# Optimization experiments

Hardware: AMD Instinct MI355X
Metric: run time of the kernel (lower is better)

Reference implementation:

```python
import jax, jax.numpy as jnp
import numpy as np

N = 100000        # nodes
E = 1600000       # edges
F_IN = 128        # input features
H = 64            # hidden
B = 256           # graphs in batch
MIN_SCORE = 1e-3  # SAGPooling min_score
TOL = 1e-7        # PyG topk tolerance
NEG = jnp.float32(-1e30)


def setup_inputs() -> dict:
    key = jax.random.key(0)
    ks = jax.random.split(key, 24)
    x = jax.random.normal(ks[0], (N, F_IN), jnp.float32)
    src = jax.random.randint(ks[1], (E,), 0, N, dtype=jnp.int32)
    dst = jax.random.randint(ks[2], (E,), 0, N, dtype=jnp.int32)
    batch = jnp.sort(jax.random.randint(ks[3], (N,), 0, B, dtype=jnp.int32))
    node_attention = jax.random.uniform(ks[4], (N,), jnp.float32)

    def lin(k, i, o):
        return jax.random.normal(k, (i, o), jnp.float32) / np.float32(np.sqrt(i))

    p = {
        'W11': lin(ks[5], F_IN, H), 'b11': jnp.zeros((H,), jnp.float32),
        'W12': lin(ks[6], H, H),    'b12': jnp.zeros((H,), jnp.float32),
        'gW1': lin(ks[7], H, 1),    'gb1': jnp.zeros((1,), jnp.float32),
        'W21': lin(ks[8], H, H),    'b21': jnp.zeros((H,), jnp.float32),
        'W22': lin(ks[9], H, H),    'b22': jnp.zeros((H,), jnp.float32),
        'gW2': lin(ks[10], H, 1),   'gb2': jnp.zeros((1,), jnp.float32),
        'W31': lin(ks[11], H, H),   'b31': jnp.zeros((H,), jnp.float32),
        'W32': lin(ks[12], H, H),   'b32': jnp.zeros((H,), jnp.float32),
        'Wl':  lin(ks[13], H, 1),   'bl': jnp.zeros((1,), jnp.float32),
    }
    return dict(x=x, src=src, dst=dst, batch=batch, node_attention=node_attention, **p)


def gin_conv(x, src, dst, emask, W1, b1, W2, b2):
    # GINConv, eps=0: mlp(x + sum_{j in N(i)} x_j), edges masked by emask
    agg = jax.ops.segment_sum(x[src] * emask[:, None], dst, num_segments=N)
    h = x + agg
    return jax.nn.relu(h @ W1 + b1) @ W2 + b2


def gcn_attn(x, src, dst, emask, nmask, W, b):
    # GCNConv(H,1) with self-loops + symmetric normalization on the masked graph
    h = x @ W  # [N,1]
    deg = jax.ops.segment_sum(emask, dst, num_segments=N) + nmask
    dinv = jnp.where(deg > 0, jax.lax.rsqrt(jnp.maximum(deg, 1e-12)), 0.0)
    coef = dinv[src] * dinv[dst] * emask
    out = jax.ops.segment_sum(h[src] * coef[:, None], dst, num_segments=N)
    out = out + h * (dinv * dinv * nmask)[:, None] + b
    return out[:, 0]


def seg_softmax(a, batch, nmask):
    am = jnp.where(nmask > 0, a, NEG)
    m = jax.ops.segment_max(am, batch, num_segments=B)
    e = jnp.where(nmask > 0, jnp.exp(a - m[batch]), 0.0)
    s = jax.ops.segment_sum(e, batch, num_segments=B)
    return e / jnp.maximum(s[batch], 1e-30)


def sag_pool(x, src, dst, emask, nmask, batch, W, b):
    attn = gcn_attn(x, src, dst, emask, nmask, W, b)
    score = seg_softmax(attn, batch, nmask)
    smax = jax.ops.segment_max(jnp.where(nmask > 0, score, NEG), batch, num_segments=B)
    thr = jnp.minimum(MIN_SCORE, smax[batch] - TOL)
    keep = ((nmask > 0) & (score > thr)).astype(x.dtype)
    x2 = x * (score * keep)[:, None]          # x[perm] * score[perm], masked form
    emask2 = emask * keep[src] * keep[dst]    # filter_adj
    return x2, emask2, keep, score


def reference(x, src, dst, batch, node_attention,
              W11, b11, W12, b12, gW1, gb1,
              W21, b21, W22, b22, gW2, gb2,
              W31, b31, W32, b32, Wl, bl):
    emask = jnp.ones((E,), x.dtype)
    nmask0 = jnp.ones((N,), x.dtype)

    h = jax.nn.relu(gin_conv(x, src, dst, emask, W11, b11, W12, b12))
    h, emask, keep1, _ = sag_pool(h, src, dst, emask, nmask0, batch, gW1, gb1)

    h = jax.nn.relu(gin_conv(h, src, dst, emask, W21, b21, W22, b22))
    h, emask, keep2, score2 = sag_pool(h, src, dst, emask, keep1, batch, gW2, gb2)

    ratio = jnp.sum(keep2) / jnp.float32(N)

    h = jax.nn.relu(gin_conv(h, src, dst, emask, W31, b31, W32, b32))

    # global max pool over surviving nodes
    hm = jnp.where(keep2[:, None] > 0, h, NEG)
    g = jax.ops.segment_max(hm, batch, num_segments=B)
    out = g @ Wl + bl  # [B,1]

    # attention KL loss; perm2 indexes the pool1-compacted array (as in the source)
    r1 = jnp.clip(jnp.cumsum(keep1).astype(jnp.int32) - 1, 0, N - 1)
    t = node_attention[r1]
    logp = jnp.log(score2 + 1e-14)
    kl = jnp.where(t > 0, t * jnp.log(jnp.maximum(t, 1e-38)), 0.0) - t * logp
    kl = kl * keep2
    s = jax.ops.segment_sum(kl, batch, num_segments=B)
    c = jax.ops.segment_sum(keep2, batch, num_segments=B)
    attn_loss = s / jnp.maximum(c, 1.0)  # scatter_mean

    return out, attn_loss, ratio
```

## Files before the change

kernel.cpp:

```cpp
#include <hip/hip_runtime.h>
#include <hip/hip_fp16.h>
#include <math.h>

#define NN 100000
#define NE 1600000
#define NB 256
#define NEGF (-1e30f)
#define NSCAN_BLK ((NN + 1023) / 1024)
#define GVB 1024
#define P_SORT 256
#define NBKT 391
#define HLEN (NBKT * P_SORT)
#define HSCAN_BLK ((HLEN + 1023) / 1024)
#define BKT_CAP 6144

__global__ void k_offs_bs(const int* __restrict__ batch, int* __restrict__ offs) {
    int g = blockIdx.x * 256 + threadIdx.x;
    if (g > NB) return;
    int lo = 0, hi = NN;
    while (lo < hi) { int mid = (lo + hi) >> 1; if (batch[mid] < g) lo = mid + 1; else hi = mid; }
    offs[g] = lo;
}

__global__ void k_hist_coarse(const int* __restrict__ dst, int* __restrict__ H) {
    __shared__ int lh[NBKT];
    int p = blockIdx.x, tid = threadIdx.x;
    for (int i = tid; i < NBKT; i += 256) lh[i] = 0;
    __syncthreads();
    int c0 = p * (NE / P_SORT), c1 = c0 + NE / P_SORT;
    for (int i = c0 + tid; i < c1; i += 256) atomicAdd(&lh[dst[i] >> 8], 1);
    __syncthreads();
    for (int i = tid; i < NBKT; i += 256) H[i * P_SORT + p] = lh[i];
}
__global__ void k_iscan_blk(const int* __restrict__ in, int* __restrict__ pref,
                            int* __restrict__ bsums, int len) {
    int blk = blockIdx.x, tid = threadIdx.x;
    int base = blk * 1024;
    int vals[4], tsum = 0;
    for (int j = 0; j < 4; ++j) {
        int idx = base + tid * 4 + j;
        int v = (idx < len) ? in[idx] : 0;
        vals[j] = tsum; tsum += v;
    }
    __shared__ int sh[256];
    sh[tid] = tsum; __syncthreads();
    for (int o = 1; o < 256; o <<= 1) {
        int v = (tid >= o) ? sh[tid - o] : 0;
        __syncthreads();
        sh[tid] += v;
        __syncthreads();
    }
    int excl = sh[tid] - tsum;
    for (int j = 0; j < 4; ++j) {
        int idx = base + tid * 4 + j;
        if (idx < len) pref[idx] = excl + vals[j];
    }
    if (tid == 255) bsums[blk] = sh[255];
}
__global__ void k_iscan_mid(int* __restrict__ bsums, int nb) {
    int acc = 0;
    for (int i = 0; i < nb; ++i) { int v = bsums[i]; bsums[i] = acc; acc += v; }
}
__global__ void k_iscan_add(int* __restrict__ pref, const int* __restrict__ bsums, int len) {
    int idx = blockIdx.x * 256 + threadIdx.x;
    if (idx < len) pref[idx] += bsums[idx >> 10];
}
__global__ void k_scatter_pairs(const int* __restrict__ src, const int* __restrict__ dst,
                                const int* __restrict__ Hs, int2* __restrict__ ebuf) {
    __shared__ int curs[NBKT];
    int p = blockIdx.x, tid = threadIdx.x;
    for (int i = tid; i < NBKT; i += 256) curs[i] = Hs[i * P_SORT + p];
    __syncthreads();
    int c0 = p * (NE / P_SORT), c1 = c0 + NE / P_SORT;
    for (int i = c0 + tid; i < c1; i += 256) {
        int d = dst[i];
        int pos = atomicAdd(&curs[d >> 8], 1);
        ebuf[pos] = make_int2(src[i], d);
    }
}
__global__ void k_bucket_csr(const int2* __restrict__ ebuf, const int* __restrict__ Hs,
                             int* __restrict__ roffs, int* __restrict__ csrc) {
    __shared__ int hist2[256];
    __shared__ int curs2[256];
    __shared__ int sh[256];
    __shared__ int stage[BKT_CAP];
    int b = blockIdx.x, tid = threadIdx.x;
    int e0 = Hs[b * P_SORT];
    int e1 = (b + 1 < NBKT) ? Hs[(b + 1) * P_SORT] : NE;
    int n0 = b * 256;
    int cntb = e1 - e0;
    if (b == 0 && tid == 0) roffs[NN] = NE;
    hist2[tid] = 0;
    __syncthreads();
    for (int i = e0 + tid; i < e1; i += 256) atomicAdd(&hist2[ebuf[i].y & 255], 1);
    __syncthreads();
    int v = hist2[tid];
    sh[tid] = v; __syncthreads();
    for (int o = 1; o < 256; o <<= 1) {
        int u = (tid >= o) ? sh[tid - o] : 0;
        __syncthreads();
        sh[tid] += u;
        __syncthreads();
    }
    int excl = sh[tid] - v;
    int node = n0 + tid;
    if (node < NN) roffs[node] = e0 + excl;
    curs2[tid] = excl;
    __syncthreads();
    if (cntb <= BKT_CAP) {
        for (int i = e0 + tid; i < e1; i += 256) {
            int2 pr = ebuf[i];
            int pos = atomicAdd(&curs2[pr.y & 255], 1);
            stage[pos] = pr.x;
        }
        __syncthreads();
        for (int i = tid; i < cntb; i += 256) csrc[e0 + i] = stage[i];
    } else {
        for (int i = e0 + tid; i < e1; i += 256) {
            int2 pr = ebuf[i];
            int pos = atomicAdd(&curs2[pr.y & 255], 1);
            csrc[e0 + pos] = pr.x;
        }
    }
}

__global__ __launch_bounds__(256) void k_pre1_g(const float* __restrict__ x,
                                                const float* __restrict__ W,
                                                float* __restrict__ y) {
    __shared__ float lds[4][4 * 128];
    int tid = threadIdx.x, w = tid >> 6, l = tid & 63;
    float Wc[128];
#pragma unroll
    for (int k = 0; k < 128; ++k) Wc[k] = W[k * 64 + l];
    float* row = lds[w];
    int g = blockIdx.x * 4 + w;
    const int G = GVB * 4;
    for (int t = g; t < NN / 4; t += G) {
        int n0 = t * 4;
#pragma unroll
        for (int r = 0; r < 4; ++r) {
            row[r * 128 + l]      = x[(size_t)(n0 + r) * 128 + l];
            row[r * 128 + 64 + l] = x[(size_t)(n0 + r) * 128 + 64 + l];
        }
        __builtin_amdgcn_wave_barrier();
        float acc[4] = {0.f, 0.f, 0.f, 0.f};
#pragma unroll
        for (int k = 0; k < 128; k += 4) {
#pragma unroll
            for (int r = 0; r < 4; ++r) {
                float4 bv = *(const float4*)&row[r * 128 + k];
                acc[r] = fmaf(bv.x, Wc[k],     acc[r]);
                acc[r] = fmaf(bv.y, Wc[k + 1], acc[r]);
                acc[r] = fmaf(bv.z, Wc[k + 2], acc[r]);
                acc[r] = fmaf(bv.w, Wc[k + 3], acc[r]);
            }
        }
        __builtin_amdgcn_wave_barrier();
#pragma unroll
        for (int r = 0; r < 4; ++r) y[(size_t)(n0 + r) * 64 + l] = acc[r];
    }
}

__global__ __launch_bounds__(256) void k_pre23_h(const float* __restrict__ h,
                                                 const float* __restrict__ sk,
                                                 const float* __restrict__ W,
                                                 __half* __restrict__ yh) {
    __shared__ float lds[4][8 * 64];
    int tid = threadIdx.x, w = tid >> 6, l = tid & 63;
    float Wc[64];
#pragma unroll
    for (int k = 0; k < 64; ++k) Wc[k] = W[k * 64 + l];
    float* row = lds[w];
    int g = blockIdx.x * 4 + w;
    const int G = GVB * 4;
    for (int t = g; t < NN / 8; t += G) {
        int n0 = t * 8;
#pragma unroll
        for (int r = 0; r < 8; ++r) row[r * 64 + l] = h[(size_t)(n0 + r) * 64 + l];
        __builtin_amdgcn_wave_barrier();
        float acc[8] = {0.f, 0.f, 0.f, 0.f, 0.f, 0.f, 0.f, 0.f};
#pragma unroll
        for (int k = 0; k < 64; k += 4) {
#pragma unroll
            for (int r = 0; r < 8; ++r) {
                float4 bv = *(const float4*)&row[r * 64 + k];
                acc[r] = fmaf(bv.x, Wc[k],     acc[r]);
                acc[r] = fmaf(bv.y, Wc[k + 1], acc[r]);
                acc[r] = fmaf(bv.z, Wc[k + 2], acc[r]);
                acc[r] = fmaf(bv.w, Wc[k + 3], acc[r]);
            }
        }
        __builtin_amdgcn_wave_barrier();
#pragma unroll
        for (int r = 0; r < 8; ++r)
            yh[(size_t)(n0 + r) * 64 + l] = __float2half(acc[r] * sk[n0 + r]);
    }
}

__global__ __launch_bounds__(256) void k_post_g(const float* __restrict__ zp,
                                                const float* __restrict__ W2,
                                                const float* __restrict__ b2,
                                                const float* __restrict__ gW,
                                                const int* __restrict__ roffs,
                                                const int* __restrict__ cnt,
                                                const float* __restrict__ keep,
                                                float* __restrict__ hOut,
                                                float* __restrict__ hwd,
                                                float* __restrict__ dinv, int mode) {
    __shared__ float lds[4][8 * 64];
    int tid = threadIdx.x, w = tid >> 6, l = tid & 63;
    float Wc[64];
#pragma unroll
    for (int k = 0; k < 64; ++k) Wc[k] = W2[k * 64 + l];
    float b2v = b2[l];
    float gWv = (mode < 3) ? gW[l] : 0.f;
    float* row = lds[w];
    int g = blockIdx.x * 4 + w;
    const int G = GVB * 4;
    for (int t = g; t < NN / 8; t += G) {
        int n0 = t * 8;
#pragma unroll
        for (int r = 0; r < 8; ++r) row[r * 64 + l] = zp[(size_t)(n0 + r) * 64 + l];
        __builtin_amdgcn_wave_barrier();
        float acc[8];
#pragma unroll
        for (int r = 0; r < 8; ++r) acc[r] = b2v;
#pragma unroll
        for (int k = 0; k < 64; k += 4) {
#pragma unroll
            for (int r = 0; r < 8; ++r) {
                float4 bv = *(const float4*)&row[r * 64 + k];
                acc[r] = fmaf(bv.x, Wc[k],     acc[r]);
                acc[r] = fmaf(bv.y, Wc[k + 1], acc[r]);
                acc[r] = fmaf(bv.z, Wc[k + 2], acc[r]);
                acc[r] = fmaf(bv.w, Wc[k + 3], acc[r]);
            }
        }
        __builtin_amdgcn_wave_barrier();
#pragma unroll
        for (int r = 0; r < 8; ++r) {
            acc[r] = fmaxf(acc[r], 0.f);
            hOut[(size_t)(n0 + r) * 64 + l] = acc[r];
        }
        if (mode < 3) {
#pragma unroll
            for (int r = 0; r < 8; ++r) {
                float t2 = acc[r] * gWv;
                for (int o = 32; o > 0; o >>= 1) t2 += __shfl_down(t2, o, 64);
                if (l == 0) {
                    int n = n0 + r;
                    float di;
                    if (mode == 1) di = 1.f / sqrtf((float)(roffs[n + 1] - roffs[n]) + 1.f);
                    else di = (keep[n] != 0.f) ? 1.f / sqrtf((float)cnt[n] + 1.f) : 0.f;
                    dinv[n] = di;
                    hwd[n] = t2 * di;
                }
            }
        }
    }
}

__global__ void k_gather_y(const float* __restrict__ y, const int* __restrict__ roffs,
                           const int* __restrict__ csrc, const float* __restrict__ b1,
                           float* __restrict__ z) {
    int tid = threadIdx.x;
    int d = blockIdx.x * 8 + (tid >> 5);
    int l = tid & 31;
    const float2* y2 = (const float2*)y;
    float2 acc = y2[(size_t)d * 32 + l];
    int e0 = roffs[d], e1 = roffs[d + 1];
    int e = e0;
    for (; e + 3 < e1; e += 4) {
        int s0 = csrc[e], s1 = csrc[e + 1], s2 = csrc[e + 2], s3 = csrc[e + 3];
        float2 v0 = y2[(size_t)s0 * 32 + l];
        float2 v1 = y2[(size_t)s1 * 32 + l];
        float2 v2 = y2[(size_t)s2 * 32 + l];
        float2 v3 = y2[(size_t)s3 * 32 + l];
        acc.x += (v0.x + v1.x) + (v2.x + v3.x);
        acc.y += (v0.y + v1.y) + (v2.y + v3.y);
    }
    for (; e < e1; ++e) {
        float2 v0 = y2[(size_t)csrc[e] * 32 + l];
        acc.x += v0.x; acc.y += v0.y;
    }
    float2 o;
    o.x = fmaxf(acc.x + b1[2 * l], 0.f);
    o.y = fmaxf(acc.y + b1[2 * l + 1], 0.f);
    ((float2*)z)[(size_t)d * 32 + l] = o;
}

__global__ void k_gather_h(const __half* __restrict__ yh, const int* __restrict__ roffs,
                           const int* __restrict__ csrc, const float* __restrict__ keepd,
                           const float* __restrict__ sk, const float* __restrict__ b1,
                           float* __restrict__ z, int* __restrict__ cnt) {
    int tid = threadIdx.x;
    int d = blockIdx.x * 8 + (tid >> 5);
    int l = tid & 31;
    const __half2* y2 = (const __half2*)yh;
    __half2 sv = y2[(size_t)d * 32 + l];
    float2 acc = make_float2(__low2float(sv), __high2float(sv));
    int c = 0;
    if (!keepd || keepd[d] != 0.f) {
        int e0 = roffs[d], e1 = roffs[d + 1];
        int e = e0;
        for (; e + 3 < e1; e += 4) {
            int s0 = csrc[e], s1 = csrc[e + 1], s2 = csrc[e + 2], s3 = csrc[e + 3];
            __half2 v0 = y2[(size_t)s0 * 32 + l];
            __half2 v1 = y2[(size_t)s1 * 32 + l];
            __half2 v2 = y2[(size_t)s2 * 32 + l];
            __half2 v3 = y2[(size_t)s3 * 32 + l];
            acc.x += (__low2float(v0) + __low2float(v1)) + (__low2float(v2) + __low2float(v3));
            acc.y += (__high2float(v0) + __high2float(v1)) + (__high2float(v2) + __high2float(v3));
            if (sk) c += (sk[s0] > 0.f) + (sk[s1] > 0.f) + (sk[s2] > 0.f) + (sk[s3] > 0.f);
        }
        for (; e < e1; ++e) {
            int s0 = csrc[e];
            __half2 v0 = y2[(size_t)s0 * 32 + l];
            acc.x += __low2float(v0); acc.y += __high2float(v0);
            if (sk) c += (sk[s0] > 0.f);
        }
    }
    float2 o;
    o.x = fmaxf(acc.x + b1[2 * l], 0.f);
    o.y = fmaxf(acc.y + b1[2 * l + 1], 0.f);
    ((float2*)z)[(size_t)d * 32 + l] = o;
    if (cnt && l == 0) cnt[d] = c;
}

__global__ void k_attn(const int* __restrict__ roffs, const int* __restrict__ csrc,
                       const float* __restrict__ hwd, const float* __restrict__ dinv,
                       const float* __restrict__ gb, float* __restrict__ attn) {
    int i = blockIdx.x * 256 + threadIdx.x;
    if (i >= NN) return;
    float sum = hwd[i];
    int e0 = roffs[i], e1 = roffs[i + 1];
    for (int e = e0; e < e1; ++e) sum += hwd[csrc[e]];
    attn[i] = dinv[i] * sum + gb[0];
}

__global__ void k_softmax_pool(const float* __restrict__ attn, const float* __restrict__ nmask,
                               const int* __restrict__ offs, float* __restrict__ score,
                               float* __restrict__ keep, float* __restrict__ sk) {
    int b = blockIdx.x, tid = threadIdx.x;
    int s0 = offs[b], s1 = offs[b + 1];
    __shared__ float red[256];
    float m = NEGF;
    for (int i = s0 + tid; i < s1; i += 256) {
        float nm = nmask ? nmask[i] : 1.f;
        if (nm > 0.f) m = fmaxf(m, attn[i]);
    }
    red[tid] = m; __syncthreads();
    for (int o = 128; o > 0; o >>= 1) { if (tid < o) red[tid] = fmaxf(red[tid], red[tid + o]); __syncthreads(); }
    m = red[0]; __syncthreads();
    float s = 0.f;
    for (int i = s0 + tid; i < s1; i += 256) {
        float nm = nmask ? nmask[i] : 1.f;
        if (nm > 0.f) s += expf(attn[i] - m);
    }
    red[tid] = s; __syncthreads();
    for (int o = 128; o > 0; o >>= 1) { if (tid < o) red[tid] += red[tid + o]; __syncthreads(); }
    s = red[0]; __syncthreads();
    float sden = fmaxf(s, 1e-30f);
    float smax = NEGF;
    for (int i = s0 + tid; i < s1; i += 256) {
        float nm = nmask ? nmask[i] : 1.f;
        float sc = (nm > 0.f) ? expf(attn[i] - m) / sden : 0.f;
        score[i] = sc;
        smax = fmaxf(smax, (nm > 0.f) ? sc : NEGF);
    }
    red[tid] = smax; __syncthreads();
    for (int o = 128; o > 0; o >>= 1) { if (tid < o) red[tid] = fmaxf(red[tid], red[tid + o]); __syncthreads(); }
    smax = red[0]; __syncthreads();
    float thr = fminf(1e-3f, smax - 1e-7f);
    for (int i = s0 + tid; i < s1; i += 256) {
        float nm = nmask ? nmask[i] : 1.f;
        float sc = score[i];
        float kp = (nm > 0.f && sc > thr) ? 1.f : 0.f;
        keep[i] = kp;
        sk[i] = sc * kp;
    }
}

__global__ void k_gmax_linear(const float* __restrict__ h, const float* __restrict__ keep2,
                              const int* __restrict__ offs, const float* __restrict__ Wl,
                              const float* __restrict__ bl, float* __restrict__ out) {
    int b = blockIdx.x, tid = threadIdx.x;
    int s0 = offs[b], s1 = offs[b + 1];
    int f = tid & 63, g = tid >> 6;
    float m = NEGF;
    for (int i = s0 + g; i < s1; i += 4)
        if (keep2[i] > 0.f) m = fmaxf(m, h[(size_t)i * 64 + f]);
    __shared__ float red[256];
    red[tid] = m; __syncthreads();
    if (g == 0) {
        m = fmaxf(fmaxf(red[f], red[64 + f]), fmaxf(red[128 + f], red[192 + f]));
        float v = m * Wl[f];
        for (int o = 32; o > 0; o >>= 1) v += __shfl_down(v, o, 64);
        if (f == 0) out[b] = v + bl[0];
    }
}

__global__ void k_scan1(const float* __restrict__ keep1, int* __restrict__ prefix,
                        int* __restrict__ bsums) {
    int blk = blockIdx.x, tid = threadIdx.x;
    int base = blk * 1024;
    int vals[4], tsum = 0;
    for (int j = 0; j < 4; ++j) {
        int idx = base + tid * 4 + j;
        int v = (idx < NN && keep1[idx] > 0.f) ? 1 : 0;
        tsum += v; vals[j] = tsum;
    }
    __shared__ int sh[256];
    sh[tid] = tsum; __syncthreads();
    for (int o = 1; o < 256; o <<= 1) {
        int v = (tid >= o) ? sh[tid - o] : 0;
        __syncthreads();
        sh[tid] += v;
        __syncthreads();
    }
    int excl = sh[tid] - tsum;
    for (int j = 0; j < 4; ++j) {
        int idx = base + tid * 4 + j;
        if (idx < NN) prefix[idx] = excl + vals[j];
    }
    if (tid == 255) bsums[blk] = sh[255];
}
__global__ void k_scan3(int* __restrict__ prefix, const int* __restrict__ boffs) {
    int idx = blockIdx.x * 256 + threadIdx.x;
    if (idx < NN) prefix[idx] += boffs[idx >> 10];
}

__global__ void k_kl(const float* __restrict__ score2, const float* __restrict__ keep2,
                     const int* __restrict__ prefix, const float* __restrict__ natt,
                     const int* __restrict__ offs, float* __restrict__ out_loss,
                     float* __restrict__ c_total) {
    int b = blockIdx.x, tid = threadIdx.x;
    int s0 = offs[b], s1 = offs[b + 1];
    float s = 0.f, c = 0.f;
    for (int i = s0 + tid; i < s1; i += 256) {
        if (keep2[i] > 0.f) {
            int r1 = prefix[i] - 1;
            r1 = max(0, min(r1, NN - 1));
            float t = natt[r1];
            float logp = logf(score2[i] + 1e-14f);
            float kl = ((t > 0.f) ? t * logf(fmaxf(t, 1e-38f)) : 0.f) - t * logp;
            s += kl; c += 1.f;
        }
    }
    __shared__ float rs[256], rc[256];
    rs[tid] = s; rc[tid] = c; __syncthreads();
    for (int o = 128; o > 0; o >>= 1) {
        if (tid < o) { rs[tid] += rs[tid + o]; rc[tid] += rc[tid + o]; }
        __syncthreads();
    }
    if (tid == 0) {
        out_loss[b] = rs[0] / fmaxf(rc[0], 1.f);
        atomicAdd(c_total, rc[0]);
    }
}
__global__ void k_final(const float* __restrict__ c_total, float* __restrict__ out) {
    out[0] = c_total[0] / (float)NN;
}

extern "C" void kernel_launch(void* const* d_in, const int* in_sizes, int n_in,
                              void* d_out, int out_size, void* d_ws, size_t ws_size,
                              hipStream_t stream) {
    const float* x    = (const float*)d_in[0];
    const int*   src  = (const int*)d_in[1];
    const int*   dst  = (const int*)d_in[2];
    const int*   batch= (const int*)d_in[3];
    const float* natt = (const float*)d_in[4];
    const float* W11 = (const float*)d_in[5],  *b11 = (const float*)d_in[6];
    const float* W12 = (const float*)d_in[7],  *b12 = (const float*)d_in[8];
    const float* gW1 = (const float*)d_in[9],  *gb1 = (const float*)d_in[10];
    const float* W21 = (const float*)d_in[11], *b21 = (const float*)d_in[12];
    const float* W22 = (const float*)d_in[13], *b22 = (const float*)d_in[14];
    const float* gW2 = (const float*)d_in[15], *gb2 = (const float*)d_in[16];
    const float* W31 = (const float*)d_in[17], *b31 = (const float*)d_in[18];
    const float* W32 = (const float*)d_in[19], *b32 = (const float*)d_in[20];
    const float* Wl  = (const float*)d_in[21], *bl  = (const float*)d_in[22];
    float* out = (float*)d_out;

    float* hA     = (float*)d_ws;
    float* hB     = hA + (size_t)NN * 64;
    float* ybuf   = hB + (size_t)NN * 64;
    float* zbuf   = ybuf + (size_t)NN * 64;
    float* hwd    = zbuf + (size_t)NN * 64;
    float* dinv   = hwd + NN;
    float* attn   = dinv + NN;
    float* score1 = attn + NN;
    float* keep1  = score1 + NN;
    float* sk1    = keep1 + NN;
    float* score2 = sk1 + NN;
    float* keep2  = score2 + NN;
    float* sk2    = keep2 + NN;
    int*   prefix = (int*)(sk2 + NN);
    int*   cnt    = prefix + NN;
    int*   roffs  = cnt + NN;
    int*   csrc   = roffs + NN + 1;
    int*   offs   = csrc + NE;
    int*   bsums  = offs + NB + 1;
    float* c_total= (float*)(bsums + 128);
    int*   H      = (int*)ybuf;
    int*   Hs     = H + HLEN;
    int2*  ebuf   = (int2*)zbuf;
    __half* yh    = (__half*)ybuf;

    const int nblk_n  = (NN + 255) / 256;
    const int nblk_n8 = NN / 8;

    k_offs_bs<<<2, 256, 0, stream>>>(batch, offs);

    k_hist_coarse<<<P_SORT, 256, 0, stream>>>(dst, H);
    k_iscan_blk<<<HSCAN_BLK, 256, 0, stream>>>(H, Hs, bsums, HLEN);
    k_iscan_mid<<<1, 1, 0, stream>>>(bsums, HSCAN_BLK);
    k_iscan_add<<<(HLEN + 255) / 256, 256, 0, stream>>>(Hs, bsums, HLEN);
    k_scatter_pairs<<<P_SORT, 256, 0, stream>>>(src, dst, Hs, ebuf);
    k_bucket_csr<<<NBKT, 256, 0, stream>>>(ebuf, Hs, roffs, csrc);

    k_pre1_g<<<GVB, 256, 0, stream>>>(x, W11, ybuf);
    k_gather_y<<<nblk_n8, 256, 0, stream>>>(ybuf, roffs, csrc, b11, zbuf);
    k_post_g<<<GVB, 256, 0, stream>>>(zbuf, W12, b12, gW1, roffs, nullptr, nullptr,
                                      hA, hwd, dinv, 1);
    k_attn<<<nblk_n, 256, 0, stream>>>(roffs, csrc, hwd, dinv, gb1, attn);
    k_softmax_pool<<<NB, 256, 0, stream>>>(attn, nullptr, offs, score1, keep1, sk1);

    k_pre23_h<<<GVB, 256, 0, stream>>>(hA, sk1, W21, yh);
    k_gather_h<<<nblk_n8, 256, 0, stream>>>(yh, roffs, csrc, keep1, sk1, b21, zbuf, cnt);
    k_post_g<<<GVB, 256, 0, stream>>>(zbuf, W22, b22, gW2, roffs, cnt, keep1,
                                      hB, hwd, dinv, 2);
    k_attn<<<nblk_n, 256, 0, stream>>>(roffs, csrc, hwd, dinv, gb2, attn);
    k_softmax_pool<<<NB, 256, 0, stream>>>(attn, keep1, offs, score2, keep2, sk2);

    k_pre23_h<<<GVB, 256, 0, stream>>>(hB, sk2, W31, yh);
    k_gather_h<<<nblk_n8, 256, 0, stream>>>(yh, roffs, csrc, keep2, nullptr, b31, zbuf, nullptr);
    k_post_g<<<GVB, 256, 0, stream>>>(zbuf, W32, b32, nullptr, roffs, nullptr, nullptr,
                                      hA, nullptr, nullptr, 3);

    k_gmax_linear<<<NB, 256, 0, stream>>>(hA, keep2, offs, Wl, bl, out);

    k_scan1<<<NSCAN_BLK, 256, 0, stream>>>(keep1, prefix, bsums);
    k_iscan_mid<<<1, 1, 0, stream>>>(bsums, NSCAN_BLK);
    k_scan3<<<nblk_n, 256, 0, stream>>>(prefix, bsums);
    hipMemsetAsync(c_total, 0, sizeof(float), stream);
    k_kl<<<NB, 256, 0, stream>>>(score2, keep2, prefix, natt, offs, out + NB, c_total);
    k_final<<<1, 1, 0, stream>>>(c_total, out + 2 * NB);
}
```

Measured before the change: 551.2 us.

## Fold small launches into neighbours and widen gather kernels to 16 lanes per node

Removes the separate batch-offset binary-search kernel by running it inside block 0 of the coarse histogram kernel. Drops the single-thread serial block-sum scan kernels; each add block now reduces the preceding block sums itself in shared memory. The gather kernels use 16 lanes per destination node with float4 (fp32) or 4xhalf (fp16) loads instead of 32 lanes with 2-wide loads, giving fewer, wider memory transactions per neighbour row. The trade-off is redundant per-block reductions and fewer threads per node, which exposes less parallelism for high-degree nodes.

```diff
diff --git a/kernel.cpp b/kernel.cpp
--- a/kernel.cpp
+++ b/kernel.cpp
@@ -14,17 +14,17 @@
 #define HSCAN_BLK ((HLEN + 1023) / 1024)
 #define BKT_CAP 6144
 
-__global__ void k_offs_bs(const int* __restrict__ batch, int* __restrict__ offs) {
-    int g = blockIdx.x * 256 + threadIdx.x;
-    if (g > NB) return;
-    int lo = 0, hi = NN;
-    while (lo < hi) { int mid = (lo + hi) >> 1; if (batch[mid] < g) lo = mid + 1; else hi = mid; }
-    offs[g] = lo;
-}
-
-__global__ void k_hist_coarse(const int* __restrict__ dst, int* __restrict__ H) {
+__global__ void k_hist_coarse(const int* __restrict__ dst, const int* __restrict__ batch,
+                              int* __restrict__ offs, int* __restrict__ H) {
     __shared__ int lh[NBKT];
     int p = blockIdx.x, tid = threadIdx.x;
+    if (p == 0) {
+        for (int g = tid; g <= NB; g += 256) {
+            int lo = 0, hi = NN;
+            while (lo < hi) { int mid = (lo + hi) >> 1; if (batch[mid] < g) lo = mid + 1; else hi = mid; }
+            offs[g] = lo;
+        }
+    }
     for (int i = tid; i < NBKT; i += 256) lh[i] = 0;
     __syncthreads();
     int c0 = p * (NE / P_SORT), c1 = c0 + NE / P_SORT;
@@ -57,13 +57,16 @@
     }
     if (tid == 255) bsums[blk] = sh[255];
 }
-__global__ void k_iscan_mid(int* __restrict__ bsums, int nb) {
-    int acc = 0;
-    for (int i = 0; i < nb; ++i) { int v = bsums[i]; bsums[i] = acc; acc += v; }
-}
 __global__ void k_iscan_add(int* __restrict__ pref, const int* __restrict__ bsums, int len) {
-    int idx = blockIdx.x * 256 + threadIdx.x;
-    if (idx < len) pref[idx] += bsums[idx >> 10];
+    __shared__ int sh[256];
+    int t = threadIdx.x;
+    int sb = blockIdx.x >> 2;
+    sh[t] = (t < sb) ? bsums[t] : 0;
+    __syncthreads();
+    for (int o = 128; o > 0; o >>= 1) { if (t < o) sh[t] += sh[t + o]; __syncthreads(); }
+    int pre = sh[0];
+    int idx = blockIdx.x * 256 + t;
+    if (idx < len) pref[idx] += pre;
 }
 __global__ void k_scatter_pairs(const int* __restrict__ src, const int* __restrict__ dst,
                                 const int* __restrict__ Hs, int2* __restrict__ ebuf) {
@@ -264,29 +267,33 @@
                            const int* __restrict__ csrc, const float* __restrict__ b1,
                            float* __restrict__ z) {
     int tid = threadIdx.x;
-    int d = blockIdx.x * 8 + (tid >> 5);
-    int l = tid & 31;
-    const float2* y2 = (const float2*)y;
-    float2 acc = y2[(size_t)d * 32 + l];
+    int d = blockIdx.x * 16 + (tid >> 4);
+    int l = tid & 15;
+    const float4* y4 = (const float4*)y;
+    float4 acc = y4[(size_t)d * 16 + l];
     int e0 = roffs[d], e1 = roffs[d + 1];
     int e = e0;
     for (; e + 3 < e1; e += 4) {
         int s0 = csrc[e], s1 = csrc[e + 1], s2 = csrc[e + 2], s3 = csrc[e + 3];
-        float2 v0 = y2[(size_t)s0 * 32 + l];
-        float2 v1 = y2[(size_t)s1 * 32 + l];
-        float2 v2 = y2[(size_t)s2 * 32 + l];
-        float2 v3 = y2[(size_t)s3 * 32 + l];
+        float4 v0 = y4[(size_t)s0 * 16 + l];
+        float4 v1 = y4[(size_t)s1 * 16 + l];
+        float4 v2 = y4[(size_t)s2 * 16 + l];
+        float4 v3 = y4[(size_t)s3 * 16 + l];
         acc.x += (v0.x + v1.x) + (v2.x + v3.x);
         acc.y += (v0.y + v1.y) + (v2.y + v3.y);
+        acc.z += (v0.z + v1.z) + (v2.z + v3.z);
+        acc.w += (v0.w + v1.w) + (v2.w + v3.w);
     }
     for (; e < e1; ++e) {
-        float2 v0 = y2[(size_t)csrc[e] * 32 + l];
-        acc.x += v0.x; acc.y += v0.y;
-    }
-    float2 o;
-    o.x = fmaxf(acc.x + b1[2 * l], 0.f);
-    o.y = fmaxf(acc.y + b1[2 * l + 1], 0.f);
-    ((float2*)z)[(size_t)d * 32 + l] = o;
+        float4 v0 = y4[(size_t)csrc[e] * 16 + l];
+        acc.x += v0.x; acc.y += v0.y; acc.z += v0.z; acc.w += v0.w;
+    }
+    float4 o;
+    o.x = fmaxf(acc.x + b1[4 * l],     0.f);
+    o.y = fmaxf(acc.y + b1[4 * l + 1], 0.f);
+    o.z = fmaxf(acc.z + b1[4 * l + 2], 0.f);
+    o.w = fmaxf(acc.w + b1[4 * l + 3], 0.f);
+    ((float4*)z)[(size_t)d * 16 + l] = o;
 }
 
 __global__ void k_gather_h(const __half* __restrict__ yh, const int* __restrict__ roffs,
@@ -294,36 +301,47 @@
                            const float* __restrict__ sk, const float* __restrict__ b1,
                            float* __restrict__ z, int* __restrict__ cnt) {
     int tid = threadIdx.x;
-    int d = blockIdx.x * 8 + (tid >> 5);
-    int l = tid & 31;
-    const __half2* y2 = (const __half2*)yh;
-    __half2 sv = y2[(size_t)d * 32 + l];
-    float2 acc = make_float2(__low2float(sv), __high2float(sv));
+    int d = blockIdx.x * 16 + (tid >> 4);
+    int l = tid & 15;
+    const float2* yv = (const float2*)yh;
+    float2 raw = yv[(size_t)d * 16 + l];
+    __half2 p0 = ((const __half2*)&raw)[0], p1 = ((const __half2*)&raw)[1];
+    float4 acc = make_float4(__low2float(p0), __high2float(p0),
+                             __low2float(p1), __high2float(p1));
     int c = 0;
     if (!keepd || keepd[d] != 0.f) {
         int e0 = roffs[d], e1 = roffs[d + 1];
         int e = e0;
         for (; e + 3 < e1; e += 4) {
             int s0 = csrc[e], s1 = csrc[e + 1], s2 = csrc[e + 2], s3 = csrc[e + 3];
-            __half2 v0 = y2[(size_t)s0 * 32 + l];
-            __half2 v1 = y2[(size_t)s1 * 32 + l];
-            __half2 v2 = y2[(size_t)s2 * 32 + l];
-            __half2 v3 = y2[(size_t)s3 * 32 + l];
-            acc.x += (__low2float(v0) + __low2float(v1)) + (__low2float(v2) + __low2float(v3));
-            acc.y += (__high2float(v0) + __high2float(v1)) + (__high2float(v2) + __high2float(v3));
+            float2 r0 = yv[(size_t)s0 * 16 + l];
+            float2 r1 = yv[(size_t)s1 * 16 + l];
+            float2 r2 = yv[(size_t)s2 * 16 + l];
+            float2 r3 = yv[(size_t)s3 * 16 + l];
+#pragma unroll
+            for (int j = 0; j < 4; ++j) {
+                float2 rr = (j == 0) ? r0 : (j == 1) ? r1 : (j == 2) ? r2 : r3;
+                __half2 a0 = ((const __half2*)&rr)[0], a1 = ((const __half2*)&rr)[1];
+                acc.x += __low2float(a0); acc.y += __high2float(a0);
+                acc.z += __low2float(a1); acc.w += __high2float(a1);
+            }
             if (sk) c += (sk[s0] > 0.f) + (sk[s1] > 0.f) + (sk[s2] > 0.f) + (sk[s3] > 0.f);
         }
         for (; e < e1; ++e) {
             int s0 = csrc[e];
-            __half2 v0 = y2[(size_t)s0 * 32 + l];
-            acc.x += __low2float(v0); acc.y += __high2float(v0);
+            float2 rr = yv[(size_t)s0 * 16 + l];
+            __half2 a0 = ((const __half2*)&rr)[0], a1 = ((const __half2*)&rr)[1];
+            acc.x += __low2float(a0); acc.y += __high2float(a0);
+            acc.z += __low2float(a1); acc.w += __high2float(a1);
             if (sk) c += (sk[s0] > 0.f);
         }
     }
-    float2 o;
-    o.x = fmaxf(acc.x + b1[2 * l], 0.f);
-    o.y = fmaxf(acc.y + b1[2 * l + 1], 0.f);
-    ((float2*)z)[(size_t)d * 32 + l] = o;
+    float4 o;
+    o.x = fmaxf(acc.x + b1[4 * l],     0.f);
+    o.y = fmaxf(acc.y + b1[4 * l + 1], 0.f);
+    o.z = fmaxf(acc.z + b1[4 * l + 2], 0.f);
+    o.w = fmaxf(acc.w + b1[4 * l + 3], 0.f);
+    ((float4*)z)[(size_t)d * 16 + l] = o;
     if (cnt && l == 0) cnt[d] = c;
 }
 
@@ -425,9 +443,16 @@
     }
     if (tid == 255) bsums[blk] = sh[255];
 }
-__global__ void k_scan3(int* __restrict__ prefix, const int* __restrict__ boffs) {
-    int idx = blockIdx.x * 256 + threadIdx.x;
-    if (idx < NN) prefix[idx] += boffs[idx >> 10];
+__global__ void k_scan3(int* __restrict__ prefix, const int* __restrict__ bsums) {
+    __shared__ int sh[256];
+    int t = threadIdx.x;
+    int sb = blockIdx.x >> 2;
+    sh[t] = (t < sb) ? bsums[t] : 0;
+    __syncthreads();
+    for (int o = 128; o > 0; o >>= 1) { if (t < o) sh[t] += sh[t + o]; __syncthreads(); }
+    int pre = sh[0];
+    int idx = blockIdx.x * 256 + t;
+    if (idx < NN) prefix[idx] += pre;
 }
 
 __global__ void k_kl(const float* __restrict__ score2, const float* __restrict__ keep2,
@@ -506,41 +531,37 @@
     int2*  ebuf   = (int2*)zbuf;
     __half* yh    = (__half*)ybuf;
 
-    const int nblk_n  = (NN + 255) / 256;
-    const int nblk_n8 = NN / 8;
-
-    k_offs_bs<<<2, 256, 0, stream>>>(batch, offs);
-
-    k_hist_coarse<<<P_SORT, 256, 0, stream>>>(dst, H);
+    const int nblk_n   = (NN + 255) / 256;
+    const int nblk_n16 = NN / 16;
+
+    k_hist_coarse<<<P_SORT, 256, 0, stream>>>(dst, batch, offs, H);
     k_iscan_blk<<<HSCAN_BLK, 256, 0, stream>>>(H, Hs, bsums, HLEN);
-    k_iscan_mid<<<1, 1, 0, stream>>>(bsums, HSCAN_BLK);
     k_iscan_add<<<(HLEN + 255) / 256, 256, 0, stream>>>(Hs, bsums, HLEN);
     k_scatter_pairs<<<P_SORT, 256, 0, stream>>>(src, dst, Hs, ebuf);
     k_bucket_csr<<<NBKT, 256, 0, stream>>>(ebuf, Hs, roffs, csrc);
 
     k_pre1_g<<<GVB, 256, 0, stream>>>(x, W11, ybuf);
-    k_gather_y<<<nblk_n8, 256, 0, stream>>>(ybuf, roffs, csrc, b11, zbuf);
+    k_gather_y<<<nblk_n16, 256, 0, stream>>>(ybuf, roffs, csrc, b11, zbuf);
     k_post_g<<<GVB, 256, 0, stream>>>(zbuf, W12, b12, gW1, roffs, nullptr, nullptr,
                                       hA, hwd, dinv, 1);
     k_attn<<<nblk_n, 256, 0, stream>>>(roffs, csrc, hwd, dinv, gb1, attn);
     k_softmax_pool<<<NB, 256, 0, stream>>>(attn, nullptr, offs, score1, keep1, sk1);
 
     k_pre23_h<<<GVB, 256, 0, stream>>>(hA, sk1, W21, yh);
-    k_gather_h<<<nblk_n8, 256, 0, stream>>>(yh, roffs, csrc, keep1, sk1, b21, zbuf, cnt);
+    k_gather_h<<<nblk_n16, 256, 0, stream>>>(yh, roffs, csrc, keep1, sk1, b21, zbuf, cnt);
     k_post_g<<<GVB, 256, 0, stream>>>(zbuf, W22, b22, gW2, roffs, cnt, keep1,
                                       hB, hwd, dinv, 2);
     k_attn<<<nblk_n, 256, 0, stream>>>(roffs, csrc, hwd, dinv, gb2, attn);
     k_softmax_pool<<<NB, 256, 0, stream>>>(attn, keep1, offs, score2, keep2, sk2);
 
     k_pre23_h<<<GVB, 256, 0, stream>>>(hB, sk2, W31, yh);
-    k_gather_h<<<nblk_n8, 256, 0, stream>>>(yh, roffs, csrc, keep2, nullptr, b31, zbuf, nullptr);
+    k_gather_h<<<nblk_n16, 256, 0, stream>>>(yh, roffs, csrc, keep2, nullptr, b31, zbuf, nullptr);
     k_post_g<<<GVB, 256, 0, stream>>>(zbuf, W32, b32, nullptr, roffs, nullptr, nullptr,
                                       hA, nullptr, nullptr, 3);
 
     k_gmax_linear<<<NB, 256, 0, stream>>>(hA, keep2, offs, Wl, bl, out);
 
     k_scan1<<<NSCAN_BLK, 256, 0, stream>>>(keep1, prefix, bsums);
-    k_iscan_mid<<<1, 1, 0, stream>>>(bsums, NSCAN_BLK);
     k_scan3<<<nblk_n, 256, 0, stream>>>(prefix, bsums);
     hipMemsetAsync(c_total, 0, sizeof(float), stream);
     k_kl<<<NB, 256, 0, stream>>>(score2, keep2, prefix, natt, offs, out + NB, c_total);
```

After: 508.1 us. -7.8%, faster.
